# Kernel optimization log

Measured on AMD Instinct MI355X. Metric: run time of the kernel, lower is better.

## Reference

```python
import jax, jax.numpy as jnp
import numpy as np

N = 6144
IN_F = 128
OUT_F = 128
H = 4
OUT_PER_HEAD = OUT_F // H  # 32
ALPHA = 0.2  # leaky relu slope
NEG_BIG = -9e15


def setup_inputs() -> dict:
    key = jax.random.key(0)
    k1, k2, k3, k4 = jax.random.split(key, 4)
    h_mat = jax.random.normal(k1, (N, IN_F), dtype=jnp.float32)
    adj = (jax.random.uniform(k2, (N, N)) < 0.05).astype(jnp.float32)
    # glorot-ish scaled params
    weight = jax.random.normal(k3, (IN_F, H * OUT_PER_HEAD), dtype=jnp.float32) * (1.0 / np.sqrt(IN_F))
    att_weight = jax.random.normal(k4, (H, 2 * OUT_PER_HEAD), dtype=jnp.float32) * (1.0 / np.sqrt(OUT_PER_HEAD))
    return {"h_mat": h_mat, "adj": adj, "weight": weight, "att_weight": att_weight}


def reference(h_mat, adj, weight, att_weight):
    n = h_mat.shape[0]
    # W h : [n, H, f]
    wh = jnp.matmul(h_mat, weight).reshape(n, H, OUT_PER_HEAD)
    a_src = att_weight[:, :OUT_PER_HEAD]   # [H, f]
    a_dst = att_weight[:, OUT_PER_HEAD:]   # [H, f]
    logit_parent = jnp.einsum("nhf,hf->nh", wh, a_src)  # [n, H]
    logit_child = jnp.einsum("nhf,hf->nh", wh, a_dst)   # [n, H]
    # e_{ij,h} = leaky_relu(parent_i + child_j) : [n, n, H]
    e = jax.nn.leaky_relu(logit_parent[:, None, :] + logit_child[None, :, :], ALPHA)
    att = jnp.where(adj[..., None] > 0, e, NEG_BIG)
    att = jax.nn.softmax(att, axis=1)  # softmax over source nodes j
    # dropout is identity in inference mode (enable_dropout=False)
    h_prime = jnp.einsum("njh,jhf->nhf", att, wh)
    return h_prime.reshape(n, -1)  # concat=True -> [n, out_features]
```

## Files before the change

kernel.cpp:

```cpp
#include <hip/hip_runtime.h>
#include <hip/hip_bf16.h>
#include <stdint.h>
#include <stddef.h>

#define GN 6144
#define GH 4
#define MAXD 512

typedef float  f32x2  __attribute__((ext_vector_type(2)));
typedef float  f32x4  __attribute__((ext_vector_type(4)));
typedef float  f32x16 __attribute__((ext_vector_type(16)));
typedef __bf16 bf16x8 __attribute__((ext_vector_type(8)));

__device__ __forceinline__ float fast_exp2(float x) {
#if __has_builtin(__builtin_amdgcn_exp2f)
  return __builtin_amdgcn_exp2f(x);
#else
  return exp2f(x);
#endif
}

__global__ __launch_bounds__(256) void gat_wh(const float* __restrict__ hm,
                                              const float* __restrict__ wgt,
                                              const float* __restrict__ aw,
                                              __bf16* __restrict__ whR,
                                              float* __restrict__ lp2,
                                              float* __restrict__ lc2) {
  __shared__ float ldsC[64 * 132];
  const int t = threadIdx.x;
  const int wave = t >> 6, lane = t & 63;
  const int col = lane & 31, kg = lane >> 5;
  const int n0 = blockIdx.x * 64;
  const int rowHalf = (wave & 1) * 32;
  const int colBase = (wave >> 1) * 64;

  f32x16 acc[2];
#pragma unroll
  for (int ct = 0; ct < 2; ++ct)
#pragma unroll
    for (int i = 0; i < 16; ++i) acc[ct][i] = 0.0f;

#pragma unroll
  for (int kk = 0; kk < 8; ++kk) {
    const int k = kk * 16 + kg * 8;
    const f32x4 h0 = *(const f32x4*)(hm + (size_t)(n0 + rowHalf + col) * 128 + k);
    const f32x4 h1 = *(const f32x4*)(hm + (size_t)(n0 + rowHalf + col) * 128 + k + 4);
    bf16x8 af;
#pragma unroll
    for (int e = 0; e < 4; ++e) { af[e] = (__bf16)h0[e]; af[e + 4] = (__bf16)h1[e]; }
#pragma unroll
    for (int ct = 0; ct < 2; ++ct) {
      bf16x8 bfr;
#pragma unroll
      for (int e = 0; e < 8; ++e)
        bfr[e] = (__bf16)wgt[(size_t)(k + e) * 128 + colBase + ct * 32 + col];
      acc[ct] = __builtin_amdgcn_mfma_f32_32x32x16_bf16(af, bfr, acc[ct], 0, 0, 0);
    }
  }
#pragma unroll
  for (int ct = 0; ct < 2; ++ct)
#pragma unroll
    for (int r = 0; r < 16; ++r)
      ldsC[(rowHalf + (r & 3) + 8 * (r >> 2) + 4 * kg) * 132 + colBase + ct * 32 + col] =
          acc[ct][r];
  __syncthreads();

  {
    const int rr = t >> 2, cg = (t & 3) * 32;
    __bf16* dst = whR + (size_t)(n0 + rr) * 128 + cg;
#pragma unroll
    for (int q = 0; q < 4; ++q) {
      bf16x8 v;
#pragma unroll
      for (int e = 0; e < 8; ++e) v[e] = (__bf16)ldsC[rr * 132 + cg + q * 8 + e];
      *(bf16x8*)(dst + q * 8) = v;
    }
  }
  {
    const int nl = t & 63, h = t >> 6;
    float sp = 0.f, sd = 0.f;
#pragma unroll
    for (int f = 0; f < 32; ++f) {
      const float v = ldsC[nl * 132 + h * 32 + f];
      sp = fmaf(v, aw[h * 64 + f], sp);
      sd = fmaf(v, aw[h * 64 + 32 + f], sd);
    }
    const float LOG2E = 1.4426950408889634f;
    lp2[(n0 + nl) * GH + h] = sp * LOG2E;
    lc2[(n0 + nl) * GH + h] = sd * LOG2E;
  }
}

__global__ __launch_bounds__(256) void gat_fused(const float* __restrict__ adj,
                                                 const __bf16* __restrict__ whR,
                                                 const float* __restrict__ lp2,
                                                 const float* __restrict__ lc2,
                                                 float* __restrict__ out) {
  __shared__ unsigned short jidx[4][MAXD];
  __shared__ float els[4][256];
  const int t = threadIdx.x, wave = t >> 6, lane = t & 63;
  const int i = blockIdx.x * 4 + wave;
  const float* arow = adj + (size_t)i * GN;

  unsigned base = 0;
  f32x4 a0 = *(const f32x4*)(arow + lane * 4);
  f32x4 a1 = *(const f32x4*)(arow + 256 + lane * 4);
  for (int c = 0; c < 24; ++c) {
    f32x4 a2;
    if (c + 2 < 24) a2 = *(const f32x4*)(arow + (c + 2) * 256 + lane * 4);
#pragma unroll
    for (int s = 0; s < 4; ++s) {
      const bool p = a0[s] > 0.f;
      const unsigned long long m = __ballot(p);
      const unsigned rank = (unsigned)__popcll(m & ((1ull << lane) - 1ull));
      if (p) jidx[wave][base + rank] = (unsigned short)(c * 256 + lane * 4 + s);
      base += (unsigned)__popcll(m);
    }
    a0 = a1; a1 = a2;
  }
  const int dg = (int)base;
  for (int k = dg + lane; k < MAXD; k += 64) jidx[wave][k] = 0;

  const f32x4 lpv = *(const f32x4*)(lp2 + (size_t)i * GH);
  const int hsel = lane >> 4;
  float acc0 = 0.f, acc1 = 0.f;
  f32x2 d01 = f32x2{0.f, 0.f}, d23 = f32x2{0.f, 0.f};

  const int nch = (dg + 63) >> 6;
  for (int c = 0; c < nch; ++c) {
    const int k = c * 64 + lane;
    const bool valid = k < dg;
    const int jv = valid ? (int)jidx[wave][k] : 0;
    const f32x4 lc = *(const f32x4*)(lc2 + (size_t)jv * GH);

    f32x2 x01 = f32x2{lpv[0] + lc[0], lpv[1] + lc[1]};
    f32x2 x23 = f32x2{lpv[2] + lc[2], lpv[3] + lc[3]};
    x01 = __builtin_elementwise_max(x01, x01 * 0.2f);
    x23 = __builtin_elementwise_max(x23, x23 * 0.2f);
    const float vf = valid ? 1.f : 0.f;
    const f32x2 e01 = f32x2{fast_exp2(x01[0]), fast_exp2(x01[1])} * vf;
    const f32x2 e23 = f32x2{fast_exp2(x23[0]), fast_exp2(x23[1])} * vf;
    d01 += e01; d23 += e23;
    *(f32x4*)&els[wave][lane * 4] = f32x4{e01[0], e01[1], e23[0], e23[1]};

    const int lim = (dg - c * 64 < 64) ? (dg - c * 64) : 64;
    for (int k2 = 0; k2 < lim; k2 += 4) {
#pragma unroll
      for (int u = 0; u < 4; ++u) {
        const int jj = (int)jidx[wave][c * 64 + k2 + u];
        const unsigned wb = *(const unsigned*)(whR + (size_t)jj * 128 + lane * 2);
        const float eb = els[wave][(k2 + u) * 4 + hsel];
        const float wlo = __uint_as_float(wb << 16);
        const float whi = __uint_as_float(wb & 0xffff0000u);
        acc0 = fmaf(eb, wlo, acc0);
        acc1 = fmaf(eb, whi, acc1);
      }
    }
  }

  f32x4 dv = f32x4{d01[0], d01[1], d23[0], d23[1]};
#pragma unroll
  for (int off = 1; off < 64; off <<= 1) {
    dv[0] += __shfl_xor(dv[0], off);
    dv[1] += __shfl_xor(dv[1], off);
    dv[2] += __shfl_xor(dv[2], off);
    dv[3] += __shfl_xor(dv[3], off);
  }
  const float den = (lane & 32) ? ((lane & 16) ? dv[3] : dv[2])
                                : ((lane & 16) ? dv[1] : dv[0]);
  const float inv = 1.0f / den;
  const f32x2 o = f32x2{acc0 * inv, acc1 * inv};
  *(f32x2*)(out + (size_t)i * 128 + lane * 2) = o;
}

extern "C" void kernel_launch(void* const* d_in, const int* in_sizes, int n_in,
                              void* d_out, int out_size, void* d_ws, size_t ws_size,
                              hipStream_t stream) {
  const float* hm  = (const float*)d_in[0];
  const float* adj = (const float*)d_in[1];
  const float* wgt = (const float*)d_in[2];
  const float* aw  = (const float*)d_in[3];
  float* out = (float*)d_out;

  char* ws = (char*)d_ws;
  __bf16* whR = (__bf16*)ws; ws += (size_t)GN * 128 * 2;
  float* lp2  = (float*)ws;  ws += GN * GH * 4;
  float* lc2  = (float*)ws;  ws += GN * GH * 4;

  gat_wh<<<96, 256, 0, stream>>>(hm, wgt, aw, whR, lp2, lc2);
  gat_fused<<<GN / 4, 256, 0, stream>>>(adj, whR, lp2, lc2, out);
}
```

Measured before the change: 65.19 us.

## Split each adjacency row across two waves and merge partial sums in LDS

```diff
diff --git a/kernel.cpp b/kernel.cpp
--- a/kernel.cpp
+++ b/kernel.cpp
@@ -5,7 +5,8 @@
 
 #define GN 6144
 #define GH 4
-#define MAXD 512
+#define HALF 3072
+#define MAXD2 256
 
 typedef float  f32x2  __attribute__((ext_vector_type(2)));
 typedef float  f32x4  __attribute__((ext_vector_type(4)));
@@ -96,32 +97,38 @@
                                                  const float* __restrict__ lp2,
                                                  const float* __restrict__ lc2,
                                                  float* __restrict__ out) {
-  __shared__ unsigned short jidx[4][MAXD];
+  __shared__ unsigned short jidx[4][MAXD2];
   __shared__ float els[4][256];
+  __shared__ float accx[4][64][2];
+  __shared__ float denx[4][4];
   const int t = threadIdx.x, wave = t >> 6, lane = t & 63;
-  const int i = blockIdx.x * 4 + wave;
-  const float* arow = adj + (size_t)i * GN;
+  const int row = blockIdx.x * 2 + (wave >> 1);
+  const int half = wave & 1;
+  const float* arow = adj + (size_t)row * GN + half * HALF;
 
   unsigned base = 0;
   f32x4 a0 = *(const f32x4*)(arow + lane * 4);
   f32x4 a1 = *(const f32x4*)(arow + 256 + lane * 4);
-  for (int c = 0; c < 24; ++c) {
+  for (int c = 0; c < 12; ++c) {
     f32x4 a2;
-    if (c + 2 < 24) a2 = *(const f32x4*)(arow + (c + 2) * 256 + lane * 4);
+    if (c + 2 < 12) a2 = *(const f32x4*)(arow + (c + 2) * 256 + lane * 4);
 #pragma unroll
     for (int s = 0; s < 4; ++s) {
       const bool p = a0[s] > 0.f;
       const unsigned long long m = __ballot(p);
       const unsigned rank = (unsigned)__popcll(m & ((1ull << lane) - 1ull));
-      if (p) jidx[wave][base + rank] = (unsigned short)(c * 256 + lane * 4 + s);
+      const unsigned pos = base + rank;
+      if (p && pos < MAXD2)
+        jidx[wave][pos] = (unsigned short)(half * HALF + c * 256 + lane * 4 + s);
       base += (unsigned)__popcll(m);
     }
     a0 = a1; a1 = a2;
   }
-  const int dg = (int)base;
-  for (int k = dg + lane; k < MAXD; k += 64) jidx[wave][k] = 0;
-
-  const f32x4 lpv = *(const f32x4*)(lp2 + (size_t)i * GH);
+  int dg = (int)base;
+  if (dg > MAXD2) dg = MAXD2;
+  for (int k = dg + lane; k < MAXD2; k += 64) jidx[wave][k] = 0;
+
+  const f32x4 lpv = *(const f32x4*)(lp2 + (size_t)row * GH);
   const int hsel = lane >> 4;
   float acc0 = 0.f, acc1 = 0.f;
   f32x2 d01 = f32x2{0.f, 0.f}, d23 = f32x2{0.f, 0.f};
@@ -166,11 +173,18 @@
     dv[2] += __shfl_xor(dv[2], off);
     dv[3] += __shfl_xor(dv[3], off);
   }
-  const float den = (lane & 32) ? ((lane & 16) ? dv[3] : dv[2])
-                                : ((lane & 16) ? dv[1] : dv[0]);
-  const float inv = 1.0f / den;
-  const f32x2 o = f32x2{acc0 * inv, acc1 * inv};
-  *(f32x2*)(out + (size_t)i * 128 + lane * 2) = o;
+
+  *(f32x2*)&accx[wave][lane][0] = f32x2{acc0, acc1};
+  if (lane == 0) *(f32x4*)&denx[wave][0] = dv;
+  __syncthreads();
+  if ((wave & 1) == 0) {
+    const float pa0 = accx[wave + 1][lane][0];
+    const float pa1 = accx[wave + 1][lane][1];
+    const float den = denx[wave][hsel] + denx[wave + 1][hsel];
+    const float inv = 1.0f / den;
+    const f32x2 o = f32x2{(acc0 + pa0) * inv, (acc1 + pa1) * inv};
+    *(f32x2*)(out + (size_t)row * 128 + lane * 2) = o;
+  }
 }
 
 extern "C" void kernel_launch(void* const* d_in, const int* in_sizes, int n_in,
@@ -188,5 +202,5 @@
   float* lc2  = (float*)ws;  ws += GN * GH * 4;
 
   gat_wh<<<96, 256, 0, stream>>>(hm, wgt, aw, whR, lp2, lc2);
-  gat_fused<<<GN / 4, 256, 0, stream>>>(adj, whR, lp2, lc2, out);
-}
+  gat_fused<<<GN / 2, 256, 0, stream>>>(adj, whR, lp2, lc2, out);
+}
```

New measurement: 62.96 us. 1.04x faster.
